# Performance work log

Measured on AMD Instinct MI355X. Metric: run time of the kernel, lower is better.

The kernel has to match this reference:

```python
import jax, jax.numpy as jnp
import numpy as np

N_NODES = 50000
N_EDGES = 800000
D_IN = 768
D_H = 256
N_CLASSES = 4
N_LAYERS = 3
N_GRAPHS = 64
LN_EPS = 1e-5


def setup_inputs() -> dict:
    key = jax.random.key(0)
    ks = jax.random.split(key, 12)
    x = jax.random.normal(ks[0], (N_NODES, D_IN), dtype=jnp.float32)
    edge_index = jax.random.randint(ks[1], (2, N_EDGES), 0, N_NODES)
    batch = jnp.sort(jax.random.randint(ks[2], (N_NODES,), 0, N_GRAPHS))
    s_in = 1.0 / np.sqrt(D_IN)
    s_h = 1.0 / np.sqrt(D_H)
    W_in = jax.random.normal(ks[3], (D_IN, D_H), jnp.float32) * s_in
    b_in = jnp.zeros((D_H,), jnp.float32)
    convW = jax.random.normal(ks[4], (N_LAYERS, D_H, D_H), jnp.float32) * s_h
    convB = jnp.zeros((N_LAYERS, D_H), jnp.float32)
    lnG = jnp.ones((N_LAYERS, D_H), jnp.float32)
    lnB = jnp.zeros((N_LAYERS, D_H), jnp.float32)
    clsW1 = jax.random.normal(ks[5], (D_H, D_H), jnp.float32) * s_h
    clsB1 = jnp.zeros((D_H,), jnp.float32)
    clsW2 = jax.random.normal(ks[6], (D_H, N_CLASSES), jnp.float32) * s_h
    clsB2 = jnp.zeros((N_CLASSES,), jnp.float32)
    return {"x": x, "edge_index": edge_index, "batch": batch,
            "W_in": W_in, "b_in": b_in, "convW": convW, "convB": convB,
            "lnG": lnG, "lnB": lnB, "clsW1": clsW1, "clsB1": clsB1,
            "clsW2": clsW2, "clsB2": clsB2}


def _layer_norm(h, g, b):
    mu = jnp.mean(h, axis=-1, keepdims=True)
    var = jnp.mean(jnp.square(h - mu), axis=-1, keepdims=True)
    return (h - mu) * jax.lax.rsqrt(var + LN_EPS) * g + b


def reference(x, edge_index, batch, W_in, b_in, convW, convB, lnG, lnB,
              clsW1, clsB1, clsW2, clsB2):
    N = x.shape[0]
    loops = jnp.arange(N)
    src = jnp.concatenate([edge_index[0], loops])  # self-loops (PyG GCNConv default)
    dst = jnp.concatenate([edge_index[1], loops])
    deg = jax.ops.segment_sum(jnp.ones_like(src, dtype=x.dtype), dst, num_segments=N)
    dinv = jax.lax.rsqrt(deg)  # deg >= 1 due to self-loops
    norm = dinv[src] * dinv[dst]  # symmetric GCN normalization per edge

    h = x @ W_in + b_in  # input projection -> [N, D_H]
    for i in range(N_LAYERS):
        m = h @ convW[i]  # transform then propagate
        h_new = jax.ops.segment_sum(m[src] * norm[:, None], dst, num_segments=N) + convB[i]
        h = jax.nn.relu(h_new + h)  # residual (shapes match), then ReLU
        h = _layer_norm(h, lnG[i], lnB[i])
        # dropout: identity (inference mode)

    g = jax.ops.segment_max(h, batch, num_segments=N_GRAPHS)  # global_max_pool
    z = jax.nn.relu(g @ clsW1 + clsB1)
    return z @ clsW2 + clsB2  # [N_GRAPHS, N_CLASSES]
```

## Files before the change

kernel.cpp:

```cpp
#include <hip/hip_runtime.h>
#include <hip/hip_bf16.h>
#include <math.h>

#define NNODES 50000
#define NEDGES 800000
#define DIN 768
#define DH 256
#define NCLS 4
#define NGRAPHS 64
#define SCAN_BLOCKS 196

typedef __bf16 bf16x8 __attribute__((ext_vector_type(8)));
typedef float f32x4 __attribute__((ext_vector_type(4)));

static __device__ __forceinline__ float bf2f(unsigned short u) {
    union { unsigned u32; float f; } v; v.u32 = ((unsigned)u) << 16; return v.f;
}
static __device__ __forceinline__ unsigned short f2bf(float f) {
    union { float f; unsigned u; } v; v.f = f;
    unsigned r = (v.u + 0x7fffu + ((v.u >> 16) & 1u)) >> 16;
    return (unsigned short)r;
}
static __device__ __forceinline__ void unpack8(uint4 u, float* f) {
    f[0] = bf2f((unsigned short)(u.x & 0xffff)); f[1] = bf2f((unsigned short)(u.x >> 16));
    f[2] = bf2f((unsigned short)(u.y & 0xffff)); f[3] = bf2f((unsigned short)(u.y >> 16));
    f[4] = bf2f((unsigned short)(u.z & 0xffff)); f[5] = bf2f((unsigned short)(u.z >> 16));
    f[6] = bf2f((unsigned short)(u.w & 0xffff)); f[7] = bf2f((unsigned short)(u.w >> 16));
}

__global__ void detect_dtype(const unsigned short* __restrict__ x, int* __restrict__ flag) {
    __shared__ int cnt_s;
    if (threadIdx.x == 0) cnt_s = 0;
    __syncthreads();
    int c = 0;
    for (int i = 0; i < 16; ++i) {
        float v = bf2f(x[threadIdx.x * 16 + i]);
        if (!(fabsf(v) < 1e10f)) c++;
    }
    atomicAdd(&cnt_s, c);
    __syncthreads();
    if (threadIdx.x == 0) flag[0] = (cnt_s > 32) ? 1 : 0;
}

static __device__ __forceinline__ unsigned short cload(const void* src, int i, int fp32) {
    return fp32 ? f2bf(((const float*)src)[i]) : ((const unsigned short*)src)[i];
}

__global__ void canon_small(const void* b_in, const void* convB, const void* lnG,
                            const void* lnB, const void* W1, const void* W2,
                            const void* b1, const void* b2,
                            unsigned short* __restrict__ dst, const int* __restrict__ flag) {
    int i = blockIdx.x * 256 + threadIdx.x;
    if (i >= 69380) return;
    const int fp32 = flag[0];
    int j = i;
    if (j < 256)  { dst[i] = cload(b_in, j, fp32); return; }  j -= 256;
    if (j < 768)  { dst[i] = cload(convB, j, fp32); return; } j -= 768;
    if (j < 768)  { dst[i] = cload(lnG, j, fp32); return; }   j -= 768;
    if (j < 768)  { dst[i] = cload(lnB, j, fp32); return; }   j -= 768;
    if (j < 65536){ dst[i] = cload(W1, j, fp32); return; }    j -= 65536;
    if (j < 1024) { dst[i] = cload(W2, j, fp32); return; }    j -= 1024;
    if (j < 256)  { dst[i] = cload(b1, j, fp32); return; }    j -= 256;
    dst[i] = cload(b2, j, fp32);
}

__global__ void transpose_win(const void* __restrict__ src, unsigned short* __restrict__ dst,
                              const int* __restrict__ flag) {
    int idx = blockIdx.x * 256 + threadIdx.x;
    if (idx < DIN * DH) {
        int r = idx / DH, c = idx % DH;
        dst[(size_t)c * DIN + r] = cload(src, idx, flag[0]);
    }
}
__global__ void transpose_convw(const void* __restrict__ src, unsigned short* __restrict__ dst,
                                const int* __restrict__ flag) {
    int idx = blockIdx.x * 256 + threadIdx.x;
    if (idx < 3 * DH * DH) {
        int l = idx >> 16, rc = idx & 65535;
        int r = rc >> 8, c = rc & 255;
        dst[(l << 16) + c * DH + r] = cload(src, idx, flag[0]);
    }
}

__global__ void fill_sentinel(float* out, int n) {
    int i = blockIdx.x * 256 + threadIdx.x;
    if (i < n) out[i] = 1000.0f;
}

__global__ void count_edges(const int* __restrict__ ei, int* __restrict__ cnt) {
    int e = blockIdx.x * 256 + threadIdx.x;
    if (e < NEDGES) atomicAdd(&cnt[ei[NEDGES + e]], 1);
}

__global__ void scan_local(const int* __restrict__ cnt, int* __restrict__ rowptr,
                           int* __restrict__ bsum) {
    __shared__ int tmp[256];
    int i = blockIdx.x * 256 + threadIdx.x;
    int v = (i < NNODES) ? cnt[i] : 0;
    tmp[threadIdx.x] = v;
    __syncthreads();
    for (int off = 1; off < 256; off <<= 1) {
        int a = (threadIdx.x >= off) ? tmp[threadIdx.x - off] : 0;
        __syncthreads();
        tmp[threadIdx.x] += a;
        __syncthreads();
    }
    if (i < NNODES) rowptr[i] = tmp[threadIdx.x] - v;
    if (threadIdx.x == 255) bsum[blockIdx.x] = tmp[255];
}
__global__ void scan_bsum(const int* __restrict__ bsum, int* __restrict__ boff) {
    __shared__ int tmp[256];
    int t = threadIdx.x;
    int v = (t < SCAN_BLOCKS) ? bsum[t] : 0;
    tmp[t] = v;
    __syncthreads();
    for (int off = 1; off < 256; off <<= 1) {
        int a = (t >= off) ? tmp[t - off] : 0;
        __syncthreads();
        tmp[t] += a;
        __syncthreads();
    }
    if (t < SCAN_BLOCKS) boff[t] = tmp[t] - v;
}
__global__ void scan_finish(int* __restrict__ rowptr, const int* __restrict__ boff,
                            const int* __restrict__ cnt, float* __restrict__ dinv) {
    int i = blockIdx.x * 256 + threadIdx.x;
    if (i < NNODES) {
        rowptr[i] += boff[blockIdx.x];
        dinv[i] = rsqrtf((float)(1 + cnt[i]));
    }
    if (i == 0) rowptr[NNODES] = NEDGES;
}

__global__ void fill_csr(const int* __restrict__ ei, const int* __restrict__ rowptr,
                         int* __restrict__ cursor, int* __restrict__ csrc) {
    int e = blockIdx.x * 256 + threadIdx.x;
    if (e < NEDGES) {
        int s = ei[e];
        int d = ei[NEDGES + e];
        int pos = rowptr[d] + atomicAdd(&cursor[d], 1);
        csrc[pos] = s;
    }
}

#define BM 64
#define BN 128
#define BK 32
#define LDSS 40

__global__ __launch_bounds__(256, 4) void gemm_bf16_tn(
    const void* __restrict__ Araw, const int* __restrict__ dflag, int use_flag,
    const unsigned short* __restrict__ Bt, const unsigned short* __restrict__ bias,
    unsigned short* __restrict__ C, int M, int N, int K)
{
    __shared__ unsigned short As[BM * LDSS];
    __shared__ unsigned short Bs[BN * LDSS];
    const int a_fp32 = use_flag ? dflag[0] : 0;
    const int m0 = blockIdx.x * BM;
    const int n0 = blockIdx.y * BN;
    const int t = threadIdx.x;
    const int wave = t >> 6, lane = t & 63;
    const int quad = lane >> 4, l16 = lane & 15;
    const int wm = (wave >> 1) << 5;
    const int wn = (wave & 1) << 6;
    const int arow = t >> 2;
    const int cg = t & 3;

    f32x4 acc[2][4];
#pragma unroll
    for (int i = 0; i < 2; i++)
#pragma unroll
        for (int j = 0; j < 4; j++) acc[i][j] = (f32x4){0.f, 0.f, 0.f, 0.f};

    for (int k0 = 0; k0 < K; k0 += BK) {
        const int gm = m0 + arow;
        uint4 av = make_uint4(0u, 0u, 0u, 0u);
        if (gm < M) {
            if (a_fp32) {
                const float* Af = (const float*)Araw + (size_t)gm * K + k0 + cg * 8;
                float4 f0 = *(const float4*)Af;
                float4 f1 = *(const float4*)(Af + 4);
                av.x = (unsigned)f2bf(f0.x) | ((unsigned)f2bf(f0.y) << 16);
                av.y = (unsigned)f2bf(f0.z) | ((unsigned)f2bf(f0.w) << 16);
                av.z = (unsigned)f2bf(f1.x) | ((unsigned)f2bf(f1.y) << 16);
                av.w = (unsigned)f2bf(f1.z) | ((unsigned)f2bf(f1.w) << 16);
            } else {
                av = *(const uint4*)((const unsigned short*)Araw + (size_t)gm * K + k0 + cg * 8);
            }
        }
        *(uint4*)(&As[arow * LDSS + cg * 8]) = av;
#pragma unroll
        for (int p = 0; p < 2; ++p) {
            const int row = arow + p * 64;
            const int gn = n0 + row;
            uint4 bv = *(const uint4*)(Bt + (size_t)gn * K + k0 + cg * 8);
            *(uint4*)(&Bs[row * LDSS + cg * 8]) = bv;
        }
        __syncthreads();
        bf16x8 af[2], bfv[4];
#pragma unroll
        for (int i = 0; i < 2; i++)
            af[i] = *(const bf16x8*)(&As[(wm + 16 * i + l16) * LDSS + quad * 8]);
#pragma unroll
        for (int j = 0; j < 4; j++)
            bfv[j] = *(const bf16x8*)(&Bs[(wn + 16 * j + l16) * LDSS + quad * 8]);
#pragma unroll
        for (int i = 0; i < 2; i++)
#pragma unroll
            for (int j = 0; j < 4; j++)
                acc[i][j] = __builtin_amdgcn_mfma_f32_16x16x32_bf16(af[i], bfv[j], acc[i][j], 0, 0, 0);
        __syncthreads();
    }
#pragma unroll
    for (int i = 0; i < 2; i++) {
#pragma unroll
        for (int j = 0; j < 4; j++) {
            int gc = n0 + wn + 16 * j + l16;
            float bv = bias ? bf2f(bias[gc]) : 0.f;
#pragma unroll
            for (int r = 0; r < 4; r++) {
                int gr = m0 + wm + 16 * i + quad * 4 + r;
                if (gr < M) C[(size_t)gr * N + gc] = f2bf(acc[i][j][r] + bv);
            }
        }
    }
}

__global__ __launch_bounds__(256) void aggregate_ln(
    const int* __restrict__ rowptr, const int* __restrict__ csrc,
    const float* __restrict__ dinv, const unsigned short* __restrict__ m,
    const unsigned short* __restrict__ convB,
    const unsigned short* __restrict__ lnG, const unsigned short* __restrict__ lnB,
    unsigned short* __restrict__ h)
{
    const int half = threadIdx.x >> 5;
    const int lane = threadIdx.x & 31;
    const int node = blockIdx.x * 8 + half;
    const float di = dinv[node];
    const size_t base = (size_t)node * DH + lane * 8;
    const size_t lo = lane * 8;

    float v0[8], v1[8], v2[8], v3[8];
    unpack8(*(const uint4*)(m + base), v0);
    const float selfn = di * di;
#pragma unroll
    for (int j = 0; j < 8; j++) { v0[j] *= selfn; v1[j] = 0.f; v2[j] = 0.f; v3[j] = 0.f; }

    const int kb = rowptr[node], ke = rowptr[node + 1];
    int k = kb;
    for (; k + 4 <= ke; k += 4) {
        const int s0 = csrc[k], s1 = csrc[k + 1], s2 = csrc[k + 2], s3 = csrc[k + 3];
        const uint4 r0 = *(const uint4*)(m + (size_t)s0 * DH + lo);
        const uint4 r1 = *(const uint4*)(m + (size_t)s1 * DH + lo);
        const uint4 r2 = *(const uint4*)(m + (size_t)s2 * DH + lo);
        const uint4 r3 = *(const uint4*)(m + (size_t)s3 * DH + lo);
        const float n0 = dinv[s0] * di, n1 = dinv[s1] * di;
        const float n2 = dinv[s2] * di, n3 = dinv[s3] * di;
        float t0[8], t1[8], t2[8], t3[8];
        unpack8(r0, t0); unpack8(r1, t1); unpack8(r2, t2); unpack8(r3, t3);
#pragma unroll
        for (int j = 0; j < 8; j++) {
            v0[j] += t0[j] * n0;
            v1[j] += t1[j] * n1;
            v2[j] += t2[j] * n2;
            v3[j] += t3[j] * n3;
        }
    }
    for (; k < ke; ++k) {
        const int s = csrc[k];
        const uint4 r = *(const uint4*)(m + (size_t)s * DH + lo);
        const float n = dinv[s] * di;
        float tv[8];
        unpack8(r, tv);
#pragma unroll
        for (int j = 0; j < 8; j++) v0[j] += tv[j] * n;
    }
#pragma unroll
    for (int j = 0; j < 8; j++) v0[j] += (v1[j] + v2[j]) + v3[j];

    float hv[8], cv[8];
    unpack8(*(const uint4*)(h + base), hv);
    unpack8(*(const uint4*)(convB + lo), cv);
    float s1 = 0.f, s2 = 0.f;
#pragma unroll
    for (int j = 0; j < 8; j++) {
        v0[j] = fmaxf(v0[j] + cv[j] + hv[j], 0.f);
        s1 += v0[j];
        s2 += v0[j] * v0[j];
    }
#pragma unroll
    for (int off = 16; off > 0; off >>= 1) {
        s1 += __shfl_xor(s1, off, 32);
        s2 += __shfl_xor(s2, off, 32);
    }
    const float mu = s1 * (1.f / 256.f);
    const float var = s2 * (1.f / 256.f) - mu * mu;
    const float rs = rsqrtf(var + 1e-5f);
    float gv[8], bv[8];
    unpack8(*(const uint4*)(lnG + lo), gv);
    unpack8(*(const uint4*)(lnB + lo), bv);
    unsigned short o[8];
#pragma unroll
    for (int j = 0; j < 8; j++) o[j] = f2bf((v0[j] - mu) * rs * gv[j] + bv[j]);
    uint4 outp;
    outp.x = (unsigned)o[0] | ((unsigned)o[1] << 16);
    outp.y = (unsigned)o[2] | ((unsigned)o[3] << 16);
    outp.z = (unsigned)o[4] | ((unsigned)o[5] << 16);
    outp.w = (unsigned)o[6] | ((unsigned)o[7] << 16);
    *(uint4*)(h + base) = outp;
}

__global__ void find_bounds(const int* __restrict__ batch, int* __restrict__ s) {
    int i = blockIdx.x * 256 + threadIdx.x;
    if (i >= NNODES) return;
    int b = batch[i];
    int bp = (i == 0) ? -1 : batch[i - 1];
    for (int g = bp + 1; g <= b; ++g) s[g] = i;
    if (i == NNODES - 1)
        for (int g = b + 1; g <= NGRAPHS; ++g) s[g] = NNODES;
}

#define PSPLIT 8
__global__ __launch_bounds__(256) void pool_partial(
    const unsigned short* __restrict__ h, const int* __restrict__ s,
    float* __restrict__ pg)
{
    const int b = blockIdx.x >> 3, split = blockIdx.x & 7, f = threadIdx.x;
    const int i0 = s[b], i1 = s[b + 1];
    const int len = i1 - i0;
    const int c0 = i0 + (int)(((long)len * split) >> 3);
    const int c1 = i0 + (int)(((long)len * (split + 1)) >> 3);
    float mx = -INFINITY;
    for (int i = c0; i < c1; ++i) mx = fmaxf(mx, bf2f(h[(size_t)i * DH + f]));
    pg[(size_t)blockIdx.x * DH + f] = mx;
}
__global__ __launch_bounds__(256) void pool_reduce(const float* __restrict__ pg,
                                                   float* __restrict__ g) {
    const int b = blockIdx.x, f = threadIdx.x;
    float mx = -INFINITY;
#pragma unroll
    for (int j = 0; j < PSPLIT; ++j) mx = fmaxf(mx, pg[(size_t)(b * PSPLIT + j) * DH + f]);
    g[b * DH + f] = mx;
}

__global__ __launch_bounds__(256) void classifier(
    const float* __restrict__ g, const unsigned short* __restrict__ W1,
    const unsigned short* __restrict__ b1, const unsigned short* __restrict__ W2,
    const unsigned short* __restrict__ b2, void* __restrict__ outv,
    const int* __restrict__ flag)
{
    __shared__ float gz[DH];
    __shared__ float zz[DH];
    const int b = blockIdx.x, t = threadIdx.x;
    gz[t] = g[b * DH + t];
    __syncthreads();
    float s = bf2f(b1[t]);
    for (int k = 0; k < DH; ++k) s += gz[k] * bf2f(W1[k * DH + t]);
    zz[t] = fmaxf(s, 0.f);
    __syncthreads();
    if (t < NCLS) {
        float s2 = bf2f(b2[t]);
        for (int k = 0; k < DH; ++k) s2 += zz[k] * bf2f(W2[k * NCLS + t]);
        if (flag[0]) ((float*)outv)[b * NCLS + t] = s2;
        else ((unsigned short*)outv)[b * NCLS + t] = f2bf(s2);
    }
}

extern "C" void kernel_launch(void* const* d_in, const int* in_sizes, int n_in,
                              void* d_out, int out_size, void* d_ws, size_t ws_size,
                              hipStream_t stream)
{
    const void* x      = d_in[0];
    const int* ei      = (const int*)d_in[1];
    const int* batch   = (const int*)d_in[2];
    const void* Win    = d_in[3];
    const void* b_in   = d_in[4];
    const void* convW  = d_in[5];
    const void* convB  = d_in[6];
    const void* lnG    = d_in[7];
    const void* lnB    = d_in[8];
    const void* W1     = d_in[9];
    const void* b1     = d_in[10];
    const void* W2     = d_in[11];
    const void* b2     = d_in[12];

    char* ws = (char*)d_ws;
    unsigned short* h   = (unsigned short*)(ws + 0);
    unsigned short* m   = (unsigned short*)(ws + 25600000);
    int* csrc           = (int*)(ws + 51200000);
    int* rowptr         = (int*)(ws + 54400000);
    int* cnt            = (int*)(ws + 54600016);
    int* cursor         = (int*)(ws + 54800016);
    float* dinv         = (float*)(ws + 55000016);
    unsigned short* cw  = (unsigned short*)(ws + 55200016);
    unsigned short* WinT= (unsigned short*)(ws + 55338784);
    unsigned short* WcT = (unsigned short*)(ws + 55732000);
    float* g            = (float*)(ws + 56125216);
    float* pg           = (float*)(ws + 56190752);
    int* gb             = (int*)(ws + 56715040);
    int* bsum           = (int*)(ws + 56715312);
    int* boff           = (int*)(ws + 56716112);
    int* flag           = (int*)(ws + 56716912);
    const size_t NEED   = 56716928;
    if (ws_size < NEED) {
        fill_sentinel<<<(out_size / 2 + 255) / 256, 256, 0, stream>>>((float*)d_out, out_size / 2);
        return;
    }

    unsigned short* cBin   = cw + 0;
    unsigned short* cConvB = cw + 256;
    unsigned short* cLnG   = cw + 1024;
    unsigned short* cLnB   = cw + 1792;
    unsigned short* cW1    = cw + 2560;
    unsigned short* cW2    = cw + 68096;
    unsigned short* cB1    = cw + 69120;
    unsigned short* cB2    = cw + 69376;

    detect_dtype<<<1, 256, 0, stream>>>((const unsigned short*)x, flag);

    hipMemsetAsync(cnt, 0, 400000, stream);
    count_edges<<<(NEDGES + 255) / 256, 256, 0, stream>>>(ei, cnt);
    scan_local<<<SCAN_BLOCKS, 256, 0, stream>>>(cnt, rowptr, bsum);
    scan_bsum<<<1, 256, 0, stream>>>(bsum, boff);
    scan_finish<<<SCAN_BLOCKS, 256, 0, stream>>>(rowptr, boff, cnt, dinv);
    fill_csr<<<(NEDGES + 255) / 256, 256, 0, stream>>>(ei, rowptr, cursor, csrc);

    canon_small<<<(69380 + 255) / 256, 256, 0, stream>>>(b_in, convB, lnG, lnB, W1, W2, b1, b2, cw, flag);
    transpose_win<<<(DIN * DH + 255) / 256, 256, 0, stream>>>(Win, WinT, flag);
    transpose_convw<<<(3 * DH * DH + 255) / 256, 256, 0, stream>>>(convW, WcT, flag);

    dim3 gg((NNODES + BM - 1) / BM, DH / BN);
    gemm_bf16_tn<<<gg, 256, 0, stream>>>(x, flag, 1, WinT, cBin, h, NNODES, DH, DIN);

    for (int i = 0; i < 3; i++) {
        gemm_bf16_tn<<<gg, 256, 0, stream>>>(h, flag, 0, WcT + i * DH * DH, nullptr, m,
                                             NNODES, DH, DH);
        aggregate_ln<<<NNODES / 8, 256, 0, stream>>>(
            rowptr, csrc, dinv, m, cConvB + i * DH, cLnG + i * DH, cLnB + i * DH, h);
    }

    find_bounds<<<(NNODES + 255) / 256, 256, 0, stream>>>(batch, gb);
    pool_partial<<<NGRAPHS * PSPLIT, 256, 0, stream>>>(h, gb, pg);
    pool_reduce<<<NGRAPHS, 256, 0, stream>>>(pg, g);
    classifier<<<NGRAPHS, 256, 0, stream>>>(g, cW1, cB1, cW2, cB2, d_out, flag);
}
```

Baseline: 679.7 us.

## Double-buffer GEMM with async global-to-LDS B loads and full-width N tile

Rewrites the bf16 GEMM so each block computes a 64x256 tile covering all of N, removing the second grid column and the repeated reads of A. Shared memory is double-buffered: the next K-slice of B is fetched straight into LDS with global_load_lds, and the next A slice is prefetched into registers while the MFMAs for the current slice run. This leaves one barrier per iteration. The padded LDS rows are replaced with an XOR swizzle to avoid bank conflicts. In exchange each wave holds more accumulators (4x4 f32x4) and the occupancy hint drops to 3 blocks per CU.

```diff
diff --git a/kernel.cpp b/kernel.cpp
--- a/kernel.cpp
+++ b/kernel.cpp
@@ -26,6 +26,18 @@
     f[2] = bf2f((unsigned short)(u.y & 0xffff)); f[3] = bf2f((unsigned short)(u.y >> 16));
     f[4] = bf2f((unsigned short)(u.z & 0xffff)); f[5] = bf2f((unsigned short)(u.z >> 16));
     f[6] = bf2f((unsigned short)(u.w & 0xffff)); f[7] = bf2f((unsigned short)(u.w >> 16));
+}
+static __device__ __forceinline__ uint4 pack8f(float4 f0, float4 f1) {
+    uint4 u;
+    u.x = (unsigned)f2bf(f0.x) | ((unsigned)f2bf(f0.y) << 16);
+    u.y = (unsigned)f2bf(f0.z) | ((unsigned)f2bf(f0.w) << 16);
+    u.z = (unsigned)f2bf(f1.x) | ((unsigned)f2bf(f1.y) << 16);
+    u.w = (unsigned)f2bf(f1.z) | ((unsigned)f2bf(f1.w) << 16);
+    return u;
+}
+static __device__ __forceinline__ void gload_lds16(const void* g, void* l) {
+    __builtin_amdgcn_global_load_lds((const __attribute__((address_space(1))) void*)g,
+                                     (__attribute__((address_space(3))) void*)l, 16, 0, 0);
 }
 
 __global__ void detect_dtype(const unsigned short* __restrict__ x, int* __restrict__ flag) {
@@ -143,84 +155,118 @@
     }
 }
 
-#define BM 64
-#define BN 128
-#define BK 32
-#define LDSS 40
-
-__global__ __launch_bounds__(256, 4) void gemm_bf16_tn(
+#define GBM 64
+#define GBN 256
+#define GBK 32
+
+__global__ __launch_bounds__(256, 3) void gemm_bf16_tn(
     const void* __restrict__ Araw, const int* __restrict__ dflag, int use_flag,
     const unsigned short* __restrict__ Bt, const unsigned short* __restrict__ bias,
     unsigned short* __restrict__ C, int M, int N, int K)
 {
-    __shared__ unsigned short As[BM * LDSS];
-    __shared__ unsigned short Bs[BN * LDSS];
+    __shared__ __align__(16) unsigned short As[2][GBM * GBK];
+    __shared__ __align__(16) unsigned short Bs[2][GBN * GBK];
+
     const int a_fp32 = use_flag ? dflag[0] : 0;
-    const int m0 = blockIdx.x * BM;
-    const int n0 = blockIdx.y * BN;
+    const int m0 = blockIdx.x * GBM;
     const int t = threadIdx.x;
     const int wave = t >> 6, lane = t & 63;
     const int quad = lane >> 4, l16 = lane & 15;
-    const int wm = (wave >> 1) << 5;
-    const int wn = (wave & 1) << 6;
-    const int arow = t >> 2;
-    const int cg = t & 3;
-
-    f32x4 acc[2][4];
-#pragma unroll
-    for (int i = 0; i < 2; i++)
+    const int qs8 = (quad ^ ((l16 >> 1) & 3)) * 8;
+
+    const int ar = t >> 2;
+    const int ap_ = t & 3;
+    const int al = ap_ ^ ((ar >> 1) & 3);
+    const bool arow_ok = (m0 + ar) < M;
+    const float* abase_f = (const float*)Araw + (size_t)(m0 + ar) * K + al * 8;
+    const unsigned short* abase_h = (const unsigned short*)Araw + (size_t)(m0 + ar) * K + al * 8;
+
+    const char* bsrcb[4];
+#pragma unroll
+    for (int li = 0; li < 4; ++li) {
+        int c = wave * 256 + li * 64 + lane;
+        int r = c >> 2, p = c & 3;
+        int l = p ^ ((r >> 1) & 3);
+        bsrcb[li] = (const char*)Bt + ((size_t)r * K + l * 8) * 2;
+    }
+
+    f32x4 acc[4][4];
+#pragma unroll
+    for (int i = 0; i < 4; i++)
 #pragma unroll
         for (int j = 0; j < 4; j++) acc[i][j] = (f32x4){0.f, 0.f, 0.f, 0.f};
 
-    for (int k0 = 0; k0 < K; k0 += BK) {
-        const int gm = m0 + arow;
+    {
+#pragma unroll
+        for (int li = 0; li < 4; ++li)
+            gload_lds16(bsrcb[li], &Bs[0][(wave * 256 + li * 64) * 8]);
         uint4 av = make_uint4(0u, 0u, 0u, 0u);
-        if (gm < M) {
+        if (arow_ok) {
             if (a_fp32) {
-                const float* Af = (const float*)Araw + (size_t)gm * K + k0 + cg * 8;
-                float4 f0 = *(const float4*)Af;
-                float4 f1 = *(const float4*)(Af + 4);
-                av.x = (unsigned)f2bf(f0.x) | ((unsigned)f2bf(f0.y) << 16);
-                av.y = (unsigned)f2bf(f0.z) | ((unsigned)f2bf(f0.w) << 16);
-                av.z = (unsigned)f2bf(f1.x) | ((unsigned)f2bf(f1.y) << 16);
-                av.w = (unsigned)f2bf(f1.z) | ((unsigned)f2bf(f1.w) << 16);
+                float4 f0 = *(const float4*)abase_f;
+                float4 f1 = *(const float4*)(abase_f + 4);
+                av = pack8f(f0, f1);
             } else {
-                av = *(const uint4*)((const unsigned short*)Araw + (size_t)gm * K + k0 + cg * 8);
+                av = *(const uint4*)abase_h;
             }
         }
-        *(uint4*)(&As[arow * LDSS + cg * 8]) = av;
-#pragma unroll
-        for (int p = 0; p < 2; ++p) {
-            const int row = arow + p * 64;
-            const int gn = n0 + row;
-            uint4 bv = *(const uint4*)(Bt + (size_t)gn * K + k0 + cg * 8);
-            *(uint4*)(&Bs[row * LDSS + cg * 8]) = bv;
+        *(uint4*)(&As[0][t * 8]) = av;
+    }
+    __syncthreads();
+
+    const int nt = K / GBK;
+    for (int tt = 0; tt < nt; ++tt) {
+        const int buf = tt & 1;
+        const bool hn = (tt + 1) < nt;
+        uint4 av = make_uint4(0u, 0u, 0u, 0u);
+        float4 f0 = make_float4(0.f, 0.f, 0.f, 0.f);
+        float4 f1 = make_float4(0.f, 0.f, 0.f, 0.f);
+        if (hn) {
+            const int kk = (tt + 1) * GBK;
+#pragma unroll
+            for (int li = 0; li < 4; ++li)
+                gload_lds16(bsrcb[li] + (size_t)kk * 2,
+                            &Bs[buf ^ 1][(wave * 256 + li * 64) * 8]);
+            if (arow_ok) {
+                if (a_fp32) {
+                    f0 = *(const float4*)(abase_f + kk);
+                    f1 = *(const float4*)(abase_f + kk + 4);
+                } else {
+                    av = *(const uint4*)(abase_h + kk);
+                }
+            }
+        }
+        const unsigned short* as_ = As[buf];
+        const unsigned short* bs_ = Bs[buf];
+        bf16x8 afv[4], bfv[4];
+#pragma unroll
+        for (int i = 0; i < 4; i++)
+            afv[i] = *(const bf16x8*)(as_ + (16 * i + l16) * 32 + qs8);
+#pragma unroll
+        for (int j = 0; j < 4; j++)
+            bfv[j] = *(const bf16x8*)(bs_ + (wave * 64 + 16 * j + l16) * 32 + qs8);
+#pragma unroll
+        for (int i = 0; i < 4; i++)
+#pragma unroll
+            for (int j = 0; j < 4; j++)
+                acc[i][j] = __builtin_amdgcn_mfma_f32_16x16x32_bf16(afv[i], bfv[j], acc[i][j], 0, 0, 0);
+        if (hn) {
+            if (a_fp32 && arow_ok) av = pack8f(f0, f1);
+            *(uint4*)(&As[buf ^ 1][t * 8]) = av;
         }
         __syncthreads();
-        bf16x8 af[2], bfv[4];
-#pragma unroll
-        for (int i = 0; i < 2; i++)
-            af[i] = *(const bf16x8*)(&As[(wm + 16 * i + l16) * LDSS + quad * 8]);
-#pragma unroll
-        for (int j = 0; j < 4; j++)
-            bfv[j] = *(const bf16x8*)(&Bs[(wn + 16 * j + l16) * LDSS + quad * 8]);
-#pragma unroll
-        for (int i = 0; i < 2; i++)
-#pragma unroll
-            for (int j = 0; j < 4; j++)
-                acc[i][j] = __builtin_amdgcn_mfma_f32_16x16x32_bf16(af[i], bfv[j], acc[i][j], 0, 0, 0);
-        __syncthreads();
-    }
-#pragma unroll
-    for (int i = 0; i < 2; i++) {
-#pragma unroll
-        for (int j = 0; j < 4; j++) {
-            int gc = n0 + wn + 16 * j + l16;
-            float bv = bias ? bf2f(bias[gc]) : 0.f;
-#pragma unroll
-            for (int r = 0; r < 4; r++) {
-                int gr = m0 + wm + 16 * i + quad * 4 + r;
-                if (gr < M) C[(size_t)gr * N + gc] = f2bf(acc[i][j][r] + bv);
+    }
+
+#pragma unroll
+    for (int j = 0; j < 4; j++) {
+        const int gc = wave * 64 + 16 * j + l16;
+        const float bv = bias ? bf2f(bias[gc]) : 0.f;
+#pragma unroll
+        for (int i = 0; i < 4; i++) {
+#pragma unroll
+            for (int rr = 0; rr < 4; rr++) {
+                int gr = m0 + 16 * i + quad * 4 + rr;
+                if (gr < M) C[(size_t)gr * N + gc] = f2bf(acc[i][j][rr] + bv);
             }
         }
     }
@@ -429,7 +475,7 @@
     transpose_win<<<(DIN * DH + 255) / 256, 256, 0, stream>>>(Win, WinT, flag);
     transpose_convw<<<(3 * DH * DH + 255) / 256, 256, 0, stream>>>(convW, WcT, flag);
 
-    dim3 gg((NNODES + BM - 1) / BM, DH / BN);
+    dim3 gg((NNODES + GBM - 1) / GBM, 1);
     gemm_bf16_tn<<<gg, 256, 0, stream>>>(x, flag, 1, WinT, cBin, h, NNODES, DH, DIN);
 
     for (int i = 0; i < 3; i++) {
```

Result: no change. 689.4 us (+1.4%).
